# Optimization experiments

Measured on AMD Instinct MI355X. Metric: run time of the kernel, lower is better.

The kernel has to match this reference:

```python
import jax, jax.numpy as jnp
import numpy as np

WS = 8            # current window
PRETRAIN = 8      # pretrain window
HEADS = 8
C = 256
UNITS = C // HEADS
SHIFT = WS // 2   # shift_mode=1 -> shift_dir=[1,1], apply_shift True (H,W > WS)
EPS = 1.55e-5
LOG100 = float(np.log(100.0))

# ---- static relative-position index and log-spaced coord table (SwinV2 CPB) ----
_c = np.arange(WS)
_rel_h = _c[:, None] - _c[None, :] + (WS - 1)          # [WS,WS] in [0, 2WS-2]
REL_INDEX = (_rel_h[:, None, :, None] * (2 * WS - 1) + _rel_h[None, :, None, :]).reshape(WS * WS, WS * WS)
_r = np.arange(-(WS - 1), WS, dtype=np.float32)
_t = np.stack(np.meshgrid(_r, _r, indexing='ij'), axis=-1).reshape(-1, 2)  # [(2WS-1)^2, 2]
_t = _t / (PRETRAIN - 1) * 8.0
CPB_TABLE = np.sign(_t) * np.log2(1.0 + np.abs(_t)) / np.log2(8.0)


def _shift_mask(H, W):
    # region labels per Swin shift mask: segments (dim-WS, WS-SHIFT, SHIFT) for shift_dir=+1
    def seg(n):
        s = np.zeros(n, np.int32)
        s[n - WS:n - SHIFT] = 1
        s[n - SHIFT:] = 2
        return s
    img = seg(H)[:, None] * 3 + seg(W)[None, :] + 1      # [H,W]
    img = img.reshape(H // WS, WS, W // WS, WS).transpose(0, 2, 1, 3).reshape(-1, WS * WS)
    d = img[:, :, None] - img[:, None, :]
    return np.where(d == 0, 0.0, -100.0).astype(np.float32)  # [nW, WS^2, WS^2]

SHIFT_MASK = _shift_mask(256, 256)


def _partition(t, H, W):
    # [B,H,W,C] -> [B,nW,heads,WS^2,units]
    B = t.shape[0]
    t = t.reshape(B, H // WS, WS, W // WS, WS, HEADS, UNITS)
    t = t.transpose(0, 1, 3, 5, 2, 4, 6)
    return t.reshape(B, (H // WS) * (W // WS), HEADS, WS * WS, UNITS)


def _reverse(t, H, W):
    B = t.shape[0]
    t = t.reshape(B, H // WS, W // WS, HEADS, WS, WS, UNITS)
    t = t.transpose(0, 1, 4, 2, 5, 3, 6)
    return t.reshape(B, H, W, C)


def _l2n(t):
    return t / jnp.sqrt(jnp.maximum(jnp.sum(t * t, axis=-1, keepdims=True), EPS))


def setup_inputs():
    key = jax.random.key(0)
    ks = jax.random.split(key, 6)
    return {
        'x': jax.random.normal(ks[0], (2, 256, 256, C), jnp.float32),
        'qkv_w': jax.random.normal(ks[1], (C, 3 * C), jnp.float32) * 0.02,
        'q_bias': jnp.zeros((C,), jnp.float32),
        'v_bias': jnp.zeros((C,), jnp.float32),
        'scale': jnp.full((HEADS, 1, 1), np.log(10.0), jnp.float32),
        'cpb_w1': jax.random.normal(ks[2], (2, 512), jnp.float32) * 0.02,
        'cpb_b1': jnp.zeros((512,), jnp.float32),
        'cpb_w2': jax.random.normal(ks[3], (512, HEADS), jnp.float32) * 0.02,
        'proj_w': jax.random.normal(ks[4], (C, C), jnp.float32) * 0.02,
        'proj_b': jnp.zeros((C,), jnp.float32),
    }


def reference(x, qkv_w, q_bias, v_bias, scale, cpb_w1, cpb_b1, cpb_w2, proj_w, proj_b):
    B, H, W, _ = x.shape
    qkv = x @ qkv_w + jnp.concatenate([q_bias, jnp.zeros_like(q_bias), v_bias])
    qkv = jnp.roll(qkv, (-SHIFT, -SHIFT), axis=(1, 2))
    q, k, v = jnp.split(qkv, 3, axis=-1)
    q = _l2n(_partition(q, H, W))          # [B,nW,h,WS^2,u]
    k = _l2n(_partition(k, H, W))
    v = _partition(v, H, W)
    logit_scale = jnp.exp(jnp.minimum(scale, LOG100))  # [h,1,1]
    attn = jnp.einsum('bwhqd,bwhkd->bwhqk', q * logit_scale, k)
    # continuous relative position bias
    cpb = jax.nn.relu(jnp.asarray(CPB_TABLE) @ cpb_w1 + cpb_b1) @ cpb_w2  # [(2WS-1)^2, h]
    bias = 16.0 * jax.nn.sigmoid(cpb[REL_INDEX])                          # [WS^2,WS^2,h]
    bias = bias.transpose(2, 0, 1)                                        # [h,WS^2,WS^2]
    attn = attn + bias[None, None] + jnp.asarray(SHIFT_MASK)[None, :, None]
    attn = jax.nn.softmax(attn, axis=-1)
    out = jnp.einsum('bwhqk,bwhkd->bwhqd', attn, v)
    out = _reverse(out, H, W)
    out = jnp.roll(out, (SHIFT, SHIFT), axis=(1, 2))
    return out @ proj_w + proj_b
```

## Files before the change

### kernel.cpp

```cpp
#include <hip/hip_runtime.h>


typedef _Float16 f16;
typedef _Float16 f16x4 __attribute__((ext_vector_type(4)));
typedef _Float16 f16x8 __attribute__((ext_vector_type(8)));
typedef float f32x4 __attribute__((ext_vector_type(4)));

#define LOG100 4.6051701859880914f
#define EPS_L2 1.55e-5f

__device__ __forceinline__ int seg2(int p) { return (p >= 248) + (p >= 252); }

__global__ __launch_bounds__(512) void k_prep(
    const float* __restrict__ cpb_w1, const float* __restrict__ cpb_b1,
    const float* __restrict__ cpb_w2, const float* __restrict__ qkv_w,
    const float* __restrict__ proj_w,
    float* __restrict__ biasfrag, f16* __restrict__ w_t, f16* __restrict__ p_t)
{
    int tid = threadIdx.x;
    if (blockIdx.x == 0) {
        __shared__ float Lw1[1024];
        __shared__ float Lb1[512];
        __shared__ float Lw2[4096];
        __shared__ float part[450 * 8];
        __shared__ float cpb[225 * 8];
        #pragma unroll
        for (int i = tid; i < 1024; i += 512) Lw1[i] = cpb_w1[i];
        if (tid < 512) Lb1[tid] = cpb_b1[tid];
        #pragma unroll
        for (int i = tid; i < 4096; i += 512) Lw2[i] = cpb_w2[i];
        __syncthreads();
        {
            int e = tid >> 1, half = tid & 1;
            if (e < 225) {
                int a = e / 15, b2 = e % 15;
                float xa = (float)(a - 7) * (8.0f / 7.0f);
                float xb = (float)(b2 - 7) * (8.0f / 7.0f);
                float t0 = (xa < 0.f ? -1.f : 1.f) * log2f(1.0f + fabsf(xa)) * (1.0f / 3.0f);
                float t1 = (xb < 0.f ? -1.f : 1.f) * log2f(1.0f + fabsf(xb)) * (1.0f / 3.0f);
                float acc[8] = {0.f, 0.f, 0.f, 0.f, 0.f, 0.f, 0.f, 0.f};
                int j0 = half << 8;
                #pragma unroll 4
                for (int j = j0; j < j0 + 256; ++j) {
                    float hh = fmaxf(t0 * Lw1[j] + t1 * Lw1[512 + j] + Lb1[j], 0.0f);
                    #pragma unroll
                    for (int h = 0; h < 8; ++h) acc[h] += hh * Lw2[j * 8 + h];
                }
                #pragma unroll
                for (int h = 0; h < 8; ++h) part[tid * 8 + h] = acc[h];
            }
        }
        __syncthreads();
        if (tid < 225) {
            #pragma unroll
            for (int h = 0; h < 8; ++h)
                cpb[tid * 8 + h] = part[tid * 16 + h] + part[tid * 16 + 8 + h];
        }
        __syncthreads();
        for (int f = tid; f < 32768; f += 512) {
            int r = f & 3, lane = (f >> 2) & 63, nt = (f >> 8) & 3, mt = (f >> 10) & 3, h = (f >> 12) & 7;
            int k = mt * 16 + ((lane >> 4) << 2) + r;
            int q = nt * 16 + (lane & 15);
            int idx = ((q >> 3) - (k >> 3) + 7) * 15 + ((q & 7) - (k & 7) + 7);
            float c = cpb[idx * 8 + h];
            biasfrag[f] = 16.0f / (1.0f + expf(-c));
        }
    } else {
        int base = (blockIdx.x - 1) * 512 + tid;
        const int stride = 128 * 512;
        for (int i = base; i < 768 * 256; i += stride) {
            int n = i >> 8, k = i & 255;
            w_t[i] = (f16)qkv_w[k * 768 + n];
        }
        for (int i = base; i < 256 * 256; i += stride) {
            int n = i >> 8, k = i & 255;
            p_t[i] = (f16)proj_w[k * 256 + n];
        }
    }
}

__global__ __launch_bounds__(512, 4) void k_fused(
    const float* __restrict__ x, const f16* __restrict__ w_t,
    const float* __restrict__ q_bias, const float* __restrict__ v_bias,
    const float* __restrict__ scale, const float* __restrict__ biasfrag,
    const f16* __restrict__ p_t, const float* __restrict__ proj_b,
    float* __restrict__ out)
{
    __shared__ char L[65536];
    const int tid = threadIdx.x;
    const int lane = tid & 63;
    const int h = tid >> 6;
    const int l15 = lane & 15, g = lane >> 4;
    const int bw = blockIdx.x;
    const int win = bw & 1023, b = bw >> 10;
    const int wh = win >> 5, ww = win & 31;
    char* wb = L + 32768 + (h << 12);
    char* vtr = L + (h << 12);
    const f32x4 fz = {0.f, 0.f, 0.f, 0.f};
    const bool boundary = (wh == 31) || (ww == 31);

    {
        int pos = tid >> 3, tc = tid & 7;
        int i2 = ((wh << 3) + (pos >> 3) + 4) & 255;
        int j2 = ((ww << 3) + (pos & 7) + 4) & 255;
        const float* xr = x + ((((long)b << 8) + i2) * 256 + j2) * 256;
        int swz = (pos & 7) << 4;
        #pragma unroll
        for (int rep = 0; rep < 4; ++rep) {
            int ch = rep * 64 + tc * 8;
            float4 v0 = *reinterpret_cast<const float4*>(xr + ch);
            float4 v1 = *reinterpret_cast<const float4*>(xr + ch + 4);
            f16x8 hv = { (f16)v0.x, (f16)v0.y, (f16)v0.z, (f16)v0.w,
                         (f16)v1.x, (f16)v1.y, (f16)v1.z, (f16)v1.w };
            *reinterpret_cast<f16x8*>(L + ((pos * 512 + ch * 2) ^ swz)) = hv;
        }
    }
    __syncthreads();

    f16x8 qa[4], kb[4];

    auto qk_pass = [&](int p, float ls, bool addb, f16x8 frag[4]) {
        f32x4 acc[2][4];
        #pragma unroll
        for (int i = 0; i < 2; ++i)
            #pragma unroll
            for (int j = 0; j < 4; ++j) acc[i][j] = fz;
        #pragma unroll
        for (int ks = 0; ks < 8; ++ks) {
            f16x8 xf[4], wf[2];
            #pragma unroll
            for (int mt = 0; mt < 4; ++mt) {
                int row = mt * 16 + l15;
                xf[mt] = *reinterpret_cast<const f16x8*>(
                    L + ((row * 512 + ks * 64 + g * 16) ^ ((row & 7) << 4)));
            }
            #pragma unroll
            for (int ct = 0; ct < 2; ++ct)
                wf[ct] = *reinterpret_cast<const f16x8*>(
                    w_t + ((p << 8) + (h << 5) + ct * 16 + l15) * 256 + ks * 32 + g * 8);
            #pragma unroll
            for (int ct = 0; ct < 2; ++ct)
                #pragma unroll
                for (int mt = 0; mt < 4; ++mt)
                    acc[ct][mt] = __builtin_amdgcn_mfma_f32_16x16x32_f16(wf[ct], xf[mt], acc[ct][mt], 0, 0, 0);
        }
        float qb0[4], qb1[4];
        #pragma unroll
        for (int r = 0; r < 4; ++r) {
            qb0[r] = addb ? q_bias[(h << 5) + (g << 2) + r] : 0.f;
            qb1[r] = addb ? q_bias[(h << 5) + 16 + (g << 2) + r] : 0.f;
        }
        #pragma unroll
        for (int nt = 0; nt < 4; ++nt) {
            int pix = nt * 16 + l15;
            float t0[4], t1[4], s2 = 0.f;
            #pragma unroll
            for (int r = 0; r < 4; ++r) {
                t0[r] = acc[0][nt][r] + qb0[r];
                t1[r] = acc[1][nt][r] + qb1[r];
                s2 += t0[r] * t0[r] + t1[r] * t1[r];
            }
            s2 += __shfl_xor(s2, 16); s2 += __shfl_xor(s2, 32);
            float iv = ls / sqrtf(fmaxf(s2, EPS_L2));
            int sw = (pix & 7) << 4;
            f16x4 p0 = { (f16)(t0[0] * iv), (f16)(t0[1] * iv), (f16)(t0[2] * iv), (f16)(t0[3] * iv) };
            f16x4 p1 = { (f16)(t1[0] * iv), (f16)(t1[1] * iv), (f16)(t1[2] * iv), (f16)(t1[3] * iv) };
            *reinterpret_cast<f16x4*>(wb + ((pix * 64 + (g << 3)) ^ sw)) = p0;
            *reinterpret_cast<f16x4*>(wb + ((pix * 64 + 32 + (g << 3)) ^ sw)) = p1;
        }
        #pragma unroll
        for (int nt = 0; nt < 4; ++nt)
            frag[nt] = *reinterpret_cast<const f16x8*>(
                wb + (((nt * 16 + l15) * 64 + g * 16) ^ ((l15 & 7) << 4)));
    };

    qk_pass(0, __expf(fminf(scale[h], LOG100)), true, qa);
    qk_pass(1, 1.0f, false, kb);

    f16x8 vf[2][2];
    {
        f32x4 av[4][2];
        #pragma unroll
        for (int mt = 0; mt < 4; ++mt) { av[mt][0] = fz; av[mt][1] = fz; }
        #pragma unroll
        for (int ks = 0; ks < 8; ++ks) {
            f16x8 xf[4], wv[2];
            #pragma unroll
            for (int mt = 0; mt < 4; ++mt) {
                int row = mt * 16 + l15;
                xf[mt] = *reinterpret_cast<const f16x8*>(
                    L + ((row * 512 + ks * 64 + g * 16) ^ ((row & 7) << 4)));
            }
            #pragma unroll
            for (int nt = 0; nt < 2; ++nt)
                wv[nt] = *reinterpret_cast<const f16x8*>(
                    w_t + (512 + (h << 5) + nt * 16 + l15) * 256 + ks * 32 + g * 8);
            #pragma unroll
            for (int mt = 0; mt < 4; ++mt)
                #pragma unroll
                for (int nt = 0; nt < 2; ++nt)
                    av[mt][nt] = __builtin_amdgcn_mfma_f32_16x16x32_f16(xf[mt], wv[nt], av[mt][nt], 0, 0, 0);
        }
        __syncthreads();
        float b0 = v_bias[(h << 5) + l15], b1 = v_bias[(h << 5) + 16 + l15];
        #pragma unroll
        for (int mt = 0; mt < 4; ++mt)
            #pragma unroll
            for (int nt = 0; nt < 2; ++nt) {
                float bsel = nt ? b1 : b0;
                f32x4 avv = av[mt][nt];
                f16x4 pk = { (f16)(avv[0] + bsel), (f16)(avv[1] + bsel),
                             (f16)(avv[2] + bsel), (f16)(avv[3] + bsel) };
                int u = nt * 16 + l15;
                int pix0 = mt * 16 + (g << 2);
                *reinterpret_cast<f16x4*>(vtr + ((u * 128 + pix0 * 2) ^ ((u & 7) << 4))) = pk;
            }
        #pragma unroll
        for (int nt = 0; nt < 2; ++nt)
            #pragma unroll
            for (int ks = 0; ks < 2; ++ks)
                vf[nt][ks] = *reinterpret_cast<const f16x8*>(
                    vtr + (((nt * 16 + l15) * 128 + ks * 64 + g * 16) ^ ((l15 & 7) << 4)));
    }

    f16x4 oh[4][2];
    #pragma unroll
    for (int c = 0; c < 2; ++c) {
        #pragma unroll
        for (int n2 = 0; n2 < 2; ++n2) {
            const int nt = c * 2 + n2;
            const int qrow = nt * 16 + l15;
            f32x4 st[4];
            #pragma unroll
            for (int mt = 0; mt < 4; ++mt)
                st[mt] = __builtin_amdgcn_mfma_f32_16x16x32_f16(kb[mt], qa[nt], fz, 0, 0, 0);
            #pragma unroll
            for (int mt = 0; mt < 4; ++mt)
                st[mt] += *reinterpret_cast<const f32x4*>(
                    biasfrag + ((((h * 4 + mt) * 4 + nt) * 64 + lane) << 2));
            if (boundary) {
                int lq = seg2((wh << 3) + (qrow >> 3)) * 3 + seg2((ww << 3) + (qrow & 7));
                #pragma unroll
                for (int mt = 0; mt < 4; ++mt)
                    #pragma unroll
                    for (int r = 0; r < 4; ++r) {
                        int k = mt * 16 + (g << 2) + r;
                        int lk = seg2((wh << 3) + (k >> 3)) * 3 + seg2((ww << 3) + (k & 7));
                        if (lq != lk) st[mt][r] -= 100.0f;
                    }
            }
            float mx = st[0][0];
            #pragma unroll
            for (int mt = 0; mt < 4; ++mt)
                #pragma unroll
                for (int r = 0; r < 4; ++r) mx = fmaxf(mx, st[mt][r]);
            mx = fmaxf(mx, __shfl_xor(mx, 16));
            mx = fmaxf(mx, __shfl_xor(mx, 32));
            float sm = 0.f;
            #pragma unroll
            for (int mt = 0; mt < 4; ++mt)
                #pragma unroll
                for (int r = 0; r < 4; ++r) {
                    float e = __expf(st[mt][r] - mx);
                    st[mt][r] = e;
                    sm += e;
                }
            sm += __shfl_xor(sm, 16);
            sm += __shfl_xor(sm, 32);
            float inv = 1.0f / sm;
            int sw = (qrow & 7) << 4;
            int rowb = (qrow & 31) * 128;
            #pragma unroll
            for (int mt = 0; mt < 4; ++mt) {
                f16x4 pk = { (f16)(st[mt][0] * inv), (f16)(st[mt][1] * inv),
                             (f16)(st[mt][2] * inv), (f16)(st[mt][3] * inv) };
                *reinterpret_cast<f16x4*>(wb + ((rowb + mt * 32 + (g << 3)) ^ sw)) = pk;
            }
        }
        #pragma unroll
        for (int m2 = 0; m2 < 2; ++m2) {
            const int mt = c * 2 + m2;
            int row = m2 * 16 + l15;
            int swz = (row & 7) << 4;
            f16x8 pa0 = *reinterpret_cast<const f16x8*>(wb + ((row * 128 + g * 16) ^ swz));
            f16x8 pa1 = *reinterpret_cast<const f16x8*>(wb + ((row * 128 + 64 + g * 16) ^ swz));
            #pragma unroll
            for (int nt = 0; nt < 2; ++nt) {
                f32x4 t = __builtin_amdgcn_mfma_f32_16x16x32_f16(pa0, vf[nt][0], fz, 0, 0, 0);
                t = __builtin_amdgcn_mfma_f32_16x16x32_f16(pa1, vf[nt][1], t, 0, 0, 0);
                oh[mt][nt] = f16x4{ (f16)t[0], (f16)t[1], (f16)t[2], (f16)t[3] };
            }
        }
    }

    __syncthreads();
    #pragma unroll
    for (int mt = 0; mt < 4; ++mt)
        #pragma unroll
        for (int r = 0; r < 4; ++r) {
            int q = mt * 16 + (g << 2) + r;
            #pragma unroll
            for (int nt = 0; nt < 2; ++nt) {
                int ch = (h << 5) + nt * 16 + l15;
                *reinterpret_cast<f16*>(L + ((q * 512 + ch * 2) ^ ((q & 7) << 4))) =
                    oh[mt][nt][r];
            }
        }
    __syncthreads();

    const int c0 = h << 5;
    f32x4 pc[4][2];
    #pragma unroll
    for (int mt = 0; mt < 4; ++mt) { pc[mt][0] = fz; pc[mt][1] = fz; }
    #pragma unroll
    for (int ks = 0; ks < 8; ++ks) {
        f16x8 a[4], bfr[2];
        #pragma unroll
        for (int mt = 0; mt < 4; ++mt) {
            int q = mt * 16 + l15;
            a[mt] = *reinterpret_cast<const f16x8*>(
                L + ((q * 512 + ks * 64 + g * 16) ^ ((q & 7) << 4)));
        }
        #pragma unroll
        for (int nt = 0; nt < 2; ++nt)
            bfr[nt] = *reinterpret_cast<const f16x8*>(
                p_t + (c0 + nt * 16 + l15) * 256 + ks * 32 + g * 8);
        #pragma unroll
        for (int mt = 0; mt < 4; ++mt)
            #pragma unroll
            for (int nt = 0; nt < 2; ++nt)
                pc[mt][nt] = __builtin_amdgcn_mfma_f32_16x16x32_f16(a[mt], bfr[nt], pc[mt][nt], 0, 0, 0);
    }
    float pb0 = proj_b[c0 + l15], pb1 = proj_b[c0 + 16 + l15];
    #pragma unroll
    for (int mt = 0; mt < 4; ++mt)
        #pragma unroll
        for (int r = 0; r < 4; ++r) {
            int q = mt * 16 + (g << 2) + r;
            int i = ((wh << 3) + (q >> 3) + 4) & 255;
            int j = ((ww << 3) + (q & 7) + 4) & 255;
            long addr = (((long)b * 256 + i) * 256 + j) * 256;
            out[addr + c0 + l15]      = pc[mt][0][r] + pb0;
            out[addr + c0 + 16 + l15] = pc[mt][1][r] + pb1;
        }
}

extern "C" void kernel_launch(void* const* d_in, const int* in_sizes, int n_in,
                              void* d_out, int out_size, void* d_ws, size_t ws_size,
                              hipStream_t stream) {
    const float* x      = (const float*)d_in[0];
    const float* qkv_w  = (const float*)d_in[1];
    const float* q_bias = (const float*)d_in[2];
    const float* v_bias = (const float*)d_in[3];
    const float* scale  = (const float*)d_in[4];
    const float* cpb_w1 = (const float*)d_in[5];
    const float* cpb_b1 = (const float*)d_in[6];
    const float* cpb_w2 = (const float*)d_in[7];
    const float* proj_w = (const float*)d_in[8];
    const float* proj_b = (const float*)d_in[9];
    float* out = (float*)d_out;

    char* ws = (char*)d_ws;
    float* biasfrag = (float*)(ws);
    f16* w_t  = (f16*)(ws + 131072);
    f16* p_t  = (f16*)(ws + 524288);

    hipLaunchKernelGGL(k_prep, dim3(129), dim3(512), 0, stream,
                       cpb_w1, cpb_b1, cpb_w2, qkv_w, proj_w, biasfrag, w_t, p_t);
    hipLaunchKernelGGL(k_fused, dim3(2048), dim3(512), 0, stream,
                       x, w_t, q_bias, v_bias, scale, biasfrag, p_t, proj_b, out);
}
```

Measured before the change: 268.9 us.

## Halve block to four waves, each processing two heads, and cut LDS to 48KB

The fused window-attention kernel now runs 256 threads per block, and each wave loops over two heads instead of handling one. The V transpose buffer reuses the per-wave scratch region, so shared memory drops from 64KB to 48KB. That should allow more blocks per CU and remove one block-wide sync from the V stage. In exchange, each wave keeps two heads' outputs in registers, which raises register pressure, and sched_barriers are added to bound live ranges.

```diff
diff --git a/kernel.cpp b/kernel.cpp
--- a/kernel.cpp
+++ b/kernel.cpp
@@ -79,35 +79,34 @@
     }
 }
 
-__global__ __launch_bounds__(512, 4) void k_fused(
+__global__ __launch_bounds__(256) void k_fused(
     const float* __restrict__ x, const f16* __restrict__ w_t,
     const float* __restrict__ q_bias, const float* __restrict__ v_bias,
     const float* __restrict__ scale, const float* __restrict__ biasfrag,
     const f16* __restrict__ p_t, const float* __restrict__ proj_b,
     float* __restrict__ out)
 {
-    __shared__ char L[65536];
+    __shared__ char L[49152];
     const int tid = threadIdx.x;
     const int lane = tid & 63;
-    const int h = tid >> 6;
+    const int wv = tid >> 6;
     const int l15 = lane & 15, g = lane >> 4;
     const int bw = blockIdx.x;
     const int win = bw & 1023, b = bw >> 10;
     const int wh = win >> 5, ww = win & 31;
-    char* wb = L + 32768 + (h << 12);
-    char* vtr = L + (h << 12);
+    char* wb = L + 32768 + (wv << 12);
     const f32x4 fz = {0.f, 0.f, 0.f, 0.f};
     const bool boundary = (wh == 31) || (ww == 31);
 
     {
-        int pos = tid >> 3, tc = tid & 7;
+        int pos = tid >> 2, tc = tid & 3;
         int i2 = ((wh << 3) + (pos >> 3) + 4) & 255;
         int j2 = ((ww << 3) + (pos & 7) + 4) & 255;
         const float* xr = x + ((((long)b << 8) + i2) * 256 + j2) * 256;
         int swz = (pos & 7) << 4;
         #pragma unroll
-        for (int rep = 0; rep < 4; ++rep) {
-            int ch = rep * 64 + tc * 8;
+        for (int rep = 0; rep < 8; ++rep) {
+            int ch = rep * 32 + tc * 8;
             float4 v0 = *reinterpret_cast<const float4*>(xr + ch);
             float4 v1 = *reinterpret_cast<const float4*>(xr + ch + 4);
             f16x8 hv = { (f16)v0.x, (f16)v0.y, (f16)v0.z, (f16)v0.w,
@@ -117,9 +116,7 @@
     }
     __syncthreads();
 
-    f16x8 qa[4], kb[4];
-
-    auto qk_pass = [&](int p, float ls, bool addb, f16x8 frag[4]) {
+    auto qk_pass = [&](int p, int h, float ls, bool addb, f16x8 frag[4]) {
         f32x4 acc[2][4];
         #pragma unroll
         for (int i = 0; i < 2; ++i)
@@ -174,175 +171,191 @@
                 wb + (((nt * 16 + l15) * 64 + g * 16) ^ ((l15 & 7) << 4)));
     };
 
-    qk_pass(0, __expf(fminf(scale[h], LOG100)), true, qa);
-    qk_pass(1, 1.0f, false, kb);
-
-    f16x8 vf[2][2];
-    {
-        f32x4 av[4][2];
-        #pragma unroll
-        for (int mt = 0; mt < 4; ++mt) { av[mt][0] = fz; av[mt][1] = fz; }
-        #pragma unroll
-        for (int ks = 0; ks < 8; ++ks) {
-            f16x8 xf[4], wv[2];
-            #pragma unroll
-            for (int mt = 0; mt < 4; ++mt) {
-                int row = mt * 16 + l15;
-                xf[mt] = *reinterpret_cast<const f16x8*>(
-                    L + ((row * 512 + ks * 64 + g * 16) ^ ((row & 7) << 4)));
-            }
+    f16x4 oh[2][4][2];
+
+    #pragma unroll
+    for (int hh = 0; hh < 2; ++hh) {
+        const int h = hh * 4 + wv;
+        f16x8 qa[4], kb[4], vf[2][2];
+
+        qk_pass(0, h, __expf(fminf(scale[h], LOG100)), true, qa);
+        __builtin_amdgcn_sched_barrier(0);
+        qk_pass(1, h, 1.0f, false, kb);
+        __builtin_amdgcn_sched_barrier(0);
+
+        {
+            f32x4 av[4][2];
+            #pragma unroll
+            for (int mt = 0; mt < 4; ++mt) { av[mt][0] = fz; av[mt][1] = fz; }
+            #pragma unroll
+            for (int ks = 0; ks < 8; ++ks) {
+                f16x8 xf[4], wv2[2];
+                #pragma unroll
+                for (int mt = 0; mt < 4; ++mt) {
+                    int row = mt * 16 + l15;
+                    xf[mt] = *reinterpret_cast<const f16x8*>(
+                        L + ((row * 512 + ks * 64 + g * 16) ^ ((row & 7) << 4)));
+                }
+                #pragma unroll
+                for (int nt = 0; nt < 2; ++nt)
+                    wv2[nt] = *reinterpret_cast<const f16x8*>(
+                        w_t + (512 + (h << 5) + nt * 16 + l15) * 256 + ks * 32 + g * 8);
+                #pragma unroll
+                for (int mt = 0; mt < 4; ++mt)
+                    #pragma unroll
+                    for (int nt = 0; nt < 2; ++nt)
+                        av[mt][nt] = __builtin_amdgcn_mfma_f32_16x16x32_f16(xf[mt], wv2[nt], av[mt][nt], 0, 0, 0);
+            }
+            float b0 = v_bias[(h << 5) + l15], b1 = v_bias[(h << 5) + 16 + l15];
+            #pragma unroll
+            for (int mt = 0; mt < 4; ++mt)
+                #pragma unroll
+                for (int nt = 0; nt < 2; ++nt) {
+                    float bsel = nt ? b1 : b0;
+                    f32x4 avv = av[mt][nt];
+                    f16x4 pk = { (f16)(avv[0] + bsel), (f16)(avv[1] + bsel),
+                                 (f16)(avv[2] + bsel), (f16)(avv[3] + bsel) };
+                    int u = nt * 16 + l15;
+                    int pix0 = mt * 16 + (g << 2);
+                    *reinterpret_cast<f16x4*>(wb + ((u * 128 + pix0 * 2) ^ ((u & 7) << 4))) = pk;
+                }
             #pragma unroll
             for (int nt = 0; nt < 2; ++nt)
-                wv[nt] = *reinterpret_cast<const f16x8*>(
-                    w_t + (512 + (h << 5) + nt * 16 + l15) * 256 + ks * 32 + g * 8);
-            #pragma unroll
-            for (int mt = 0; mt < 4; ++mt)
-                #pragma unroll
-                for (int nt = 0; nt < 2; ++nt)
-                    av[mt][nt] = __builtin_amdgcn_mfma_f32_16x16x32_f16(xf[mt], wv[nt], av[mt][nt], 0, 0, 0);
-        }
-        __syncthreads();
-        float b0 = v_bias[(h << 5) + l15], b1 = v_bias[(h << 5) + 16 + l15];
-        #pragma unroll
-        for (int mt = 0; mt < 4; ++mt)
-            #pragma unroll
-            for (int nt = 0; nt < 2; ++nt) {
-                float bsel = nt ? b1 : b0;
-                f32x4 avv = av[mt][nt];
-                f16x4 pk = { (f16)(avv[0] + bsel), (f16)(avv[1] + bsel),
-                             (f16)(avv[2] + bsel), (f16)(avv[3] + bsel) };
-                int u = nt * 16 + l15;
-                int pix0 = mt * 16 + (g << 2);
-                *reinterpret_cast<f16x4*>(vtr + ((u * 128 + pix0 * 2) ^ ((u & 7) << 4))) = pk;
-            }
-        #pragma unroll
-        for (int nt = 0; nt < 2; ++nt)
-            #pragma unroll
-            for (int ks = 0; ks < 2; ++ks)
-                vf[nt][ks] = *reinterpret_cast<const f16x8*>(
-                    vtr + (((nt * 16 + l15) * 128 + ks * 64 + g * 16) ^ ((l15 & 7) << 4)));
-    }
-
-    f16x4 oh[4][2];
-    #pragma unroll
-    for (int c = 0; c < 2; ++c) {
-        #pragma unroll
-        for (int n2 = 0; n2 < 2; ++n2) {
-            const int nt = c * 2 + n2;
-            const int qrow = nt * 16 + l15;
-            f32x4 st[4];
-            #pragma unroll
-            for (int mt = 0; mt < 4; ++mt)
-                st[mt] = __builtin_amdgcn_mfma_f32_16x16x32_f16(kb[mt], qa[nt], fz, 0, 0, 0);
-            #pragma unroll
-            for (int mt = 0; mt < 4; ++mt)
-                st[mt] += *reinterpret_cast<const f32x4*>(
-                    biasfrag + ((((h * 4 + mt) * 4 + nt) * 64 + lane) << 2));
-            if (boundary) {
-                int lq = seg2((wh << 3) + (qrow >> 3)) * 3 + seg2((ww << 3) + (qrow & 7));
+                #pragma unroll
+                for (int ks = 0; ks < 2; ++ks)
+                    vf[nt][ks] = *reinterpret_cast<const f16x8*>(
+                        wb + (((nt * 16 + l15) * 128 + ks * 64 + g * 16) ^ ((l15 & 7) << 4)));
+        }
+        __builtin_amdgcn_sched_barrier(0);
+
+        #pragma unroll
+        for (int c = 0; c < 2; ++c) {
+            #pragma unroll
+            for (int n2 = 0; n2 < 2; ++n2) {
+                const int nt = c * 2 + n2;
+                const int qrow = nt * 16 + l15;
+                f32x4 st[4];
+                #pragma unroll
+                for (int mt = 0; mt < 4; ++mt)
+                    st[mt] = __builtin_amdgcn_mfma_f32_16x16x32_f16(kb[mt], qa[nt], fz, 0, 0, 0);
+                #pragma unroll
+                for (int mt = 0; mt < 4; ++mt)
+                    st[mt] += *reinterpret_cast<const f32x4*>(
+                        biasfrag + ((((h * 4 + mt) * 4 + nt) * 64 + lane) << 2));
+                if (boundary) {
+                    int lq = seg2((wh << 3) + (qrow >> 3)) * 3 + seg2((ww << 3) + (qrow & 7));
+                    #pragma unroll
+                    for (int mt = 0; mt < 4; ++mt)
+                        #pragma unroll
+                        for (int r = 0; r < 4; ++r) {
+                            int k = mt * 16 + (g << 2) + r;
+                            int lk = seg2((wh << 3) + (k >> 3)) * 3 + seg2((ww << 3) + (k & 7));
+                            if (lq != lk) st[mt][r] -= 100.0f;
+                        }
+                }
+                float mx = st[0][0];
+                #pragma unroll
+                for (int mt = 0; mt < 4; ++mt)
+                    #pragma unroll
+                    for (int r = 0; r < 4; ++r) mx = fmaxf(mx, st[mt][r]);
+                mx = fmaxf(mx, __shfl_xor(mx, 16));
+                mx = fmaxf(mx, __shfl_xor(mx, 32));
+                float sm = 0.f;
                 #pragma unroll
                 for (int mt = 0; mt < 4; ++mt)
                     #pragma unroll
                     for (int r = 0; r < 4; ++r) {
-                        int k = mt * 16 + (g << 2) + r;
-                        int lk = seg2((wh << 3) + (k >> 3)) * 3 + seg2((ww << 3) + (k & 7));
-                        if (lq != lk) st[mt][r] -= 100.0f;
+                        float e = __expf(st[mt][r] - mx);
+                        st[mt][r] = e;
+                        sm += e;
                     }
-            }
-            float mx = st[0][0];
-            #pragma unroll
-            for (int mt = 0; mt < 4; ++mt)
-                #pragma unroll
-                for (int r = 0; r < 4; ++r) mx = fmaxf(mx, st[mt][r]);
-            mx = fmaxf(mx, __shfl_xor(mx, 16));
-            mx = fmaxf(mx, __shfl_xor(mx, 32));
-            float sm = 0.f;
-            #pragma unroll
-            for (int mt = 0; mt < 4; ++mt)
-                #pragma unroll
-                for (int r = 0; r < 4; ++r) {
-                    float e = __expf(st[mt][r] - mx);
-                    st[mt][r] = e;
-                    sm += e;
-                }
-            sm += __shfl_xor(sm, 16);
-            sm += __shfl_xor(sm, 32);
-            float inv = 1.0f / sm;
-            int sw = (qrow & 7) << 4;
-            int rowb = (qrow & 31) * 128;
-            #pragma unroll
-            for (int mt = 0; mt < 4; ++mt) {
-                f16x4 pk = { (f16)(st[mt][0] * inv), (f16)(st[mt][1] * inv),
-                             (f16)(st[mt][2] * inv), (f16)(st[mt][3] * inv) };
-                *reinterpret_cast<f16x4*>(wb + ((rowb + mt * 32 + (g << 3)) ^ sw)) = pk;
-            }
-        }
-        #pragma unroll
-        for (int m2 = 0; m2 < 2; ++m2) {
-            const int mt = c * 2 + m2;
-            int row = m2 * 16 + l15;
-            int swz = (row & 7) << 4;
-            f16x8 pa0 = *reinterpret_cast<const f16x8*>(wb + ((row * 128 + g * 16) ^ swz));
-            f16x8 pa1 = *reinterpret_cast<const f16x8*>(wb + ((row * 128 + 64 + g * 16) ^ swz));
-            #pragma unroll
-            for (int nt = 0; nt < 2; ++nt) {
-                f32x4 t = __builtin_amdgcn_mfma_f32_16x16x32_f16(pa0, vf[nt][0], fz, 0, 0, 0);
-                t = __builtin_amdgcn_mfma_f32_16x16x32_f16(pa1, vf[nt][1], t, 0, 0, 0);
-                oh[mt][nt] = f16x4{ (f16)t[0], (f16)t[1], (f16)t[2], (f16)t[3] };
-            }
-        }
+                sm += __shfl_xor(sm, 16);
+                sm += __shfl_xor(sm, 32);
+                float inv = 1.0f / sm;
+                int sw = (qrow & 7) << 4;
+                int rowb = (qrow & 31) * 128;
+                #pragma unroll
+                for (int mt = 0; mt < 4; ++mt) {
+                    f16x4 pk = { (f16)(st[mt][0] * inv), (f16)(st[mt][1] * inv),
+                                 (f16)(st[mt][2] * inv), (f16)(st[mt][3] * inv) };
+                    *reinterpret_cast<f16x4*>(wb + ((rowb + mt * 32 + (g << 3)) ^ sw)) = pk;
+                }
+            }
+            #pragma unroll
+            for (int m2 = 0; m2 < 2; ++m2) {
+                const int mt = c * 2 + m2;
+                int row = m2 * 16 + l15;
+                int swz = (row & 7) << 4;
+                f16x8 pa0 = *reinterpret_cast<const f16x8*>(wb + ((row * 128 + g * 16) ^ swz));
+                f16x8 pa1 = *reinterpret_cast<const f16x8*>(wb + ((row * 128 + 64 + g * 16) ^ swz));
+                #pragma unroll
+                for (int nt = 0; nt < 2; ++nt) {
+                    f32x4 t = __builtin_amdgcn_mfma_f32_16x16x32_f16(pa0, vf[nt][0], fz, 0, 0, 0);
+                    t = __builtin_amdgcn_mfma_f32_16x16x32_f16(pa1, vf[nt][1], t, 0, 0, 0);
+                    oh[hh][mt][nt] = f16x4{ (f16)t[0], (f16)t[1], (f16)t[2], (f16)t[3] };
+                }
+            }
+        }
+        __builtin_amdgcn_sched_barrier(0);
     }
 
     __syncthreads();
     #pragma unroll
-    for (int mt = 0; mt < 4; ++mt)
-        #pragma unroll
-        for (int r = 0; r < 4; ++r) {
-            int q = mt * 16 + (g << 2) + r;
-            #pragma unroll
-            for (int nt = 0; nt < 2; ++nt) {
-                int ch = (h << 5) + nt * 16 + l15;
-                *reinterpret_cast<f16*>(L + ((q * 512 + ch * 2) ^ ((q & 7) << 4))) =
-                    oh[mt][nt][r];
-            }
-        }
+    for (int hh = 0; hh < 2; ++hh) {
+        const int h = hh * 4 + wv;
+        #pragma unroll
+        for (int mt = 0; mt < 4; ++mt)
+            #pragma unroll
+            for (int r = 0; r < 4; ++r) {
+                int q = mt * 16 + (g << 2) + r;
+                #pragma unroll
+                for (int nt = 0; nt < 2; ++nt) {
+                    int ch = (h << 5) + nt * 16 + l15;
+                    *reinterpret_cast<f16*>(L + ((q * 512 + ch * 2) ^ ((q & 7) << 4))) =
+                        oh[hh][mt][nt][r];
+                }
+            }
+    }
     __syncthreads();
 
-    const int c0 = h << 5;
-    f32x4 pc[4][2];
-    #pragma unroll
-    for (int mt = 0; mt < 4; ++mt) { pc[mt][0] = fz; pc[mt][1] = fz; }
-    #pragma unroll
-    for (int ks = 0; ks < 8; ++ks) {
-        f16x8 a[4], bfr[2];
-        #pragma unroll
-        for (int mt = 0; mt < 4; ++mt) {
-            int q = mt * 16 + l15;
-            a[mt] = *reinterpret_cast<const f16x8*>(
-                L + ((q * 512 + ks * 64 + g * 16) ^ ((q & 7) << 4)));
-        }
-        #pragma unroll
-        for (int nt = 0; nt < 2; ++nt)
-            bfr[nt] = *reinterpret_cast<const f16x8*>(
-                p_t + (c0 + nt * 16 + l15) * 256 + ks * 32 + g * 8);
+    #pragma unroll 1
+    for (int sp = 0; sp < 2; ++sp) {
+        const int c0 = ((sp * 4 + wv) << 5);
+        f32x4 pc[4][2];
+        #pragma unroll
+        for (int mt = 0; mt < 4; ++mt) { pc[mt][0] = fz; pc[mt][1] = fz; }
+        #pragma unroll
+        for (int ks = 0; ks < 8; ++ks) {
+            f16x8 a[4], bfr[2];
+            #pragma unroll
+            for (int mt = 0; mt < 4; ++mt) {
+                int q = mt * 16 + l15;
+                a[mt] = *reinterpret_cast<const f16x8*>(
+                    L + ((q * 512 + ks * 64 + g * 16) ^ ((q & 7) << 4)));
+            }
+            #pragma unroll
+            for (int nt = 0; nt < 2; ++nt)
+                bfr[nt] = *reinterpret_cast<const f16x8*>(
+                    p_t + (c0 + nt * 16 + l15) * 256 + ks * 32 + g * 8);
+            #pragma unroll
+            for (int mt = 0; mt < 4; ++mt)
+                #pragma unroll
+                for (int nt = 0; nt < 2; ++nt)
+                    pc[mt][nt] = __builtin_amdgcn_mfma_f32_16x16x32_f16(a[mt], bfr[nt], pc[mt][nt], 0, 0, 0);
+        }
+        float pb0 = proj_b[c0 + l15], pb1 = proj_b[c0 + 16 + l15];
         #pragma unroll
         for (int mt = 0; mt < 4; ++mt)
             #pragma unroll
-            for (int nt = 0; nt < 2; ++nt)
-                pc[mt][nt] = __builtin_amdgcn_mfma_f32_16x16x32_f16(a[mt], bfr[nt], pc[mt][nt], 0, 0, 0);
-    }
-    float pb0 = proj_b[c0 + l15], pb1 = proj_b[c0 + 16 + l15];
-    #pragma unroll
-    for (int mt = 0; mt < 4; ++mt)
-        #pragma unroll
-        for (int r = 0; r < 4; ++r) {
-            int q = mt * 16 + (g << 2) + r;
-            int i = ((wh << 3) + (q >> 3) + 4) & 255;
-            int j = ((ww << 3) + (q & 7) + 4) & 255;
-            long addr = (((long)b * 256 + i) * 256 + j) * 256;
-            out[addr + c0 + l15]      = pc[mt][0][r] + pb0;
-            out[addr + c0 + 16 + l15] = pc[mt][1][r] + pb1;
-        }
+            for (int r = 0; r < 4; ++r) {
+                int q = mt * 16 + (g << 2) + r;
+                int i = ((wh << 3) + (q >> 3) + 4) & 255;
+                int j = ((ww << 3) + (q & 7) + 4) & 255;
+                long addr = (((long)b * 256 + i) * 256 + j) * 256;
+                out[addr + c0 + l15]      = pc[mt][0][r] + pb0;
+                out[addr + c0 + 16 + l15] = pc[mt][1][r] + pb1;
+            }
+    }
 }
 
 extern "C" void kernel_launch(void* const* d_in, const int* in_sizes, int n_in,
@@ -367,6 +380,6 @@
 
     hipLaunchKernelGGL(k_prep, dim3(129), dim3(512), 0, stream,
                        cpb_w1, cpb_b1, cpb_w2, qkv_w, proj_w, biasfrag, w_t, p_t);
-    hipLaunchKernelGGL(k_fused, dim3(2048), dim3(512), 0, stream,
+    hipLaunchKernelGGL(k_fused, dim3(2048), dim3(256), 0, stream,
                        x, w_t, q_bias, v_bias, scale, biasfrag, p_t, proj_b, out);
 }
```

New measurement: 308.8 us. 14.8% more time.
